# Optimization experiments

Measured on AMD Instinct MI355X. Metric: run time of the kernel, lower is better.

Reference implementation:

```python
import jax, jax.numpy as jnp
import numpy as np


def setup_inputs() -> dict:
    key = jax.random.key(0)
    kq, kk, kv, kiq, kik = jax.random.split(key, 5)
    B, H, S, D = 2, 16, 4096, 64
    NSQ = 2048  # round(0.5 * S)
    NSK = 2048  # round(0.5 * S)
    Q = jax.random.normal(kq, (B, H, S, D), dtype=jnp.float32)
    K = jax.random.normal(kk, (B, H, S, D), dtype=jnp.float32)
    V = jax.random.normal(kv, (B, H, S, D), dtype=jnp.float32)
    mask = jnp.ones((B, S), dtype=jnp.float32)
    sample_idx_q = jnp.sort(jax.random.randint(kiq, (NSQ,), 0, S, dtype=jnp.int32))
    sample_idx_k = jax.random.randint(kik, (NSK,), 0, S, dtype=jnp.int32)
    return {"Q": Q, "K": K, "V": V, "mask": mask,
            "sample_idx_q": sample_idx_q, "sample_idx_k": sample_idx_k}


def reference(Q, K, V, mask, sample_idx_q, sample_idx_k):
    # Q,K,V: [B,H,S,D]; sample_idx_q sorted int [NSQ]; sample_idx_k int [NSK]
    S = Q.shape[-2]
    nsq = sample_idx_q.shape[0]
    nsk = sample_idx_k.shape[0]
    Qs = Q[:, :, sample_idx_q, :]            # [B,H,NSQ,D]
    Vs = V[:, :, sample_idx_k, :]            # [B,H,NSK,D]
    # NOTE: original code computes K's softmax from Q (faithful to source bug):
    Qsm = jax.nn.softmax(Qs, axis=-1)        # softmax over head_dim
    Ksm = jax.nn.softmax(Qsm, axis=-2)       # softmax over sampled seq dim
    # dot = K^T @ V : [B,H,D,D]  (requires NSQ == NSK, as in source)
    dot = jnp.einsum('bhsd,bhse->bhde', Ksm, Vs)
    ac = jnp.einsum('bhsd,bhde->bhse', Qsm, dot)  # [B,H,NSQ,D]
    scale = (S * S) / (nsq * nsk)
    ac = scale * ac + (S / nsk) * Vs
    # Serial duplicate-merge + scatter == segmented sum over duplicate q indices,
    # written into a zero tensor at the unique sampled positions.
    attn = jnp.zeros_like(V).at[:, :, sample_idx_q, :].add(ac)
    return attn
```

## Files before the change

### kernel.cpp

```cpp
#include <hip/hip_runtime.h>

constexpr int S     = 4096;
constexpr int D     = 64;
constexpr int NSQ   = 2048;
constexpr int BH    = 32;
constexpr int SD    = S * D;
constexpr int SPLIT = 32;
constexpr int RPB   = NSQ / SPLIT;
constexpr int RPW   = RPB / 4;
constexpr int PE    = 66;
constexpr int PQ    = 68;

using f32x16 = __attribute__((ext_vector_type(16))) float;
using s16x8  = __attribute__((ext_vector_type(8)))  short;

#define DEV static __device__ __forceinline__

DEV unsigned short f2bf(float f) {
    unsigned x = __builtin_bit_cast(unsigned, f);
    x += 0x7fffu + ((x >> 16) & 1u);
    return (unsigned short)(x >> 16);
}

DEV float row_softmax(float q) {
    float mx = q;
    #pragma unroll
    for (int s = 32; s; s >>= 1) mx = fmaxf(mx, __shfl_xor(mx, s));
    float e = __expf(q - mx);
    float sm = e;
    #pragma unroll
    for (int s = 32; s; s >>= 1) sm += __shfl_xor(sm, s);
    return e / sm;
}

DEV s16x8 load_frag(const unsigned short* p) {
    const unsigned* u = (const unsigned*)p;
    union { unsigned w[4]; s16x8 v; } r;
    r.w[0] = u[0]; r.w[1] = u[1]; r.w[2] = u[2]; r.w[3] = u[3];
    return r.v;
}

__global__ __launch_bounds__(256) void
kA(const float* __restrict__ Q, const float* __restrict__ V,
   const int* __restrict__ iq, const int* __restrict__ ik,
   float* __restrict__ Mws, float* __restrict__ Cws) {
    __shared__ unsigned short Et[64 * PE];
    __shared__ unsigned short Vt[64 * PE];
    __shared__ float Cl[4][64];

    const int bh   = blockIdx.x / SPLIT;
    const int sp   = blockIdx.x % SPLIT;
    const int lane = threadIdx.x & 63;
    const int wave = threadIdx.x >> 6;

    const float* Qb = Q + (size_t)bh * SD;
    const float* Vb = V + (size_t)bh * SD;

    float c = 0.f;
    const int rbase = sp * RPB + wave * RPW;
    #pragma unroll 2
    for (int r = 0; r < RPW; ++r) {
        const int i  = rbase + r;
        const int qi = iq[i];
        const int ki = ik[i];
        const float q = Qb[qi * D + lane];
        const float v = Vb[ki * D + lane];
        const float qsm = row_softmax(q);
        const float ev  = __expf(qsm);
        c += ev;
        const int sl = wave * RPW + r;
        Et[lane * PE + sl] = f2bf(ev);
        Vt[lane * PE + sl] = f2bf(v);
    }
    Cl[wave][lane] = c;
    __syncthreads();

    const int d0 = (wave & 1) * 32, e0 = (wave >> 1) * 32;
    const int m  = lane & 31, h = lane >> 5;
    f32x16 acc = {0,0,0,0,0,0,0,0,0,0,0,0,0,0,0,0};
    #pragma unroll
    for (int t = 0; t < RPB / 16; ++t) {
        s16x8 a = load_frag(&Et[(d0 + m) * PE + t * 16 + h * 8]);
        s16x8 b = load_frag(&Vt[(e0 + m) * PE + t * 16 + h * 8]);
        acc = __builtin_amdgcn_mfma_f32_32x32x16_bf16(a, b, acc, 0, 0, 0);
    }

    float* Mb = Mws + bh * 4096;
    #pragma unroll
    for (int r = 0; r < 16; ++r) {
        const int row = (r & 3) + 8 * (r >> 2) + 4 * h;
        atomicAdd(&Mb[(d0 + row) * 64 + (e0 + m)], acc[r]);
    }
    if (wave == 0) {
        const float cs = Cl[0][lane] + Cl[1][lane] + Cl[2][lane] + Cl[3][lane];
        atomicAdd(&Cws[bh * 64 + lane], cs);
    }
}

__global__ __launch_bounds__(256) void
kC(const float* __restrict__ Q, const float* __restrict__ V,
   const int* __restrict__ iq, const int* __restrict__ ik,
   const float* __restrict__ Mws, const float* __restrict__ Cws,
   float* __restrict__ out) {
    __shared__ unsigned short Qs[RPB * PQ];
    __shared__ unsigned short Gt[64 * PQ];
    __shared__ int iqL[RPB];
    __shared__ int ikL[RPB];

    const int bh   = blockIdx.x / SPLIT;
    const int sp   = blockIdx.x % SPLIT;
    const int lane = threadIdx.x & 63;
    const int wave = threadIdx.x >> 6;

    const float* Mb = Mws + bh * 4096;
    const float* Cb = Cws + bh * 64;
    for (int t = threadIdx.x; t < 4096; t += 256) {
        const int d = t >> 6, e = t & 63;
        Gt[e * PQ + d] = f2bf(4.0f * Mb[t] / Cb[d]);
    }

    const float* Qb = Q + (size_t)bh * SD;
    const float* Vb = V + (size_t)bh * SD;
    float*       Ob = out + (size_t)bh * SD;
    const int rbase = sp * RPB;

    if (threadIdx.x < RPB) {
        iqL[threadIdx.x] = iq[rbase + threadIdx.x];
        ikL[threadIdx.x] = ik[rbase + threadIdx.x];
    }

    #pragma unroll 2
    for (int r = 0; r < RPW; ++r) {
        const int sl = wave * RPW + r;
        const int i  = rbase + sl;
        const int qi = iq[i];
        const float q = Qb[qi * D + lane];
        Qs[sl * PQ + lane] = f2bf(row_softmax(q));
    }
    __syncthreads();

    const int m0 = (wave & 1) * 32, n0 = (wave >> 1) * 32;
    const int m  = lane & 31, h = lane >> 5;

    f32x16 acc;
    #pragma unroll
    for (int r = 0; r < 16; ++r) {
        const int row = (r & 3) + 8 * (r >> 2) + 4 * h;
        const int ki  = ikL[m0 + row];
        acc[r] = 2.0f * Vb[ki * D + n0 + m];
    }
    #pragma unroll
    for (int t = 0; t < RPB / 16; ++t) {
        s16x8 a = load_frag(&Qs[(m0 + m) * PQ + t * 16 + h * 8]);
        s16x8 b = load_frag(&Gt[(n0 + m) * PQ + t * 16 + h * 8]);
        acc = __builtin_amdgcn_mfma_f32_32x32x16_bf16(a, b, acc, 0, 0, 0);
    }
    #pragma unroll
    for (int r = 0; r < 16; ++r) {
        const int row = (r & 3) + 8 * (r >> 2) + 4 * h;
        const int qi  = iqL[m0 + row];
        atomicAdd(&Ob[qi * D + n0 + m], acc[r]);
    }
}

extern "C" void kernel_launch(void* const* d_in, const int* in_sizes, int n_in,
                              void* d_out, int out_size, void* d_ws, size_t ws_size,
                              hipStream_t stream) {
    const float* Q  = (const float*)d_in[0];
    const float* V  = (const float*)d_in[2];
    const int*   iq = (const int*)d_in[4];
    const int*   ik = (const int*)d_in[5];
    float*       out = (float*)d_out;

    float* Mws = (float*)d_ws;
    float* Cws = Mws + BH * D * D;

    hipMemsetAsync(d_out, 0, (size_t)out_size * sizeof(float), stream);
    hipMemsetAsync(d_ws, 0, (size_t)(BH * D * D + BH * D) * sizeof(float), stream);

    kA<<<BH * SPLIT, 256, 0, stream>>>(Q, V, iq, ik, Mws, Cws);
    kC<<<BH * SPLIT, 256, 0, stream>>>(Q, V, iq, ik, Mws, Cws, out);
}
```

Measured before the change: 174.5 us.

## Replace atomic K^T V accumulation with per-split partials and vectorized softmax loads

kA now writes a per-split partial D×D matrix and column sums to workspace instead of using atomicAdd. kC sums those partials itself, which removes the workspace memset and the atomic contention. Both kernels now load Q and V rows as float4 with 16 lanes per row, computing the row softmax with a 4-step shuffle reduction instead of a full 64-lane reduce. kA uses 16 splits with 128 rows each, halving its block count. The cost is that every kC block redundantly reads all 16 partials (256 KB per bh), which adds L2 traffic.

```diff
diff --git a/kernel.cpp b/kernel.cpp
--- a/kernel.cpp
+++ b/kernel.cpp
@@ -1,15 +1,22 @@
 #include <hip/hip_runtime.h>
 
-constexpr int S     = 4096;
-constexpr int D     = 64;
-constexpr int NSQ   = 2048;
-constexpr int BH    = 32;
-constexpr int SD    = S * D;
-constexpr int SPLIT = 32;
-constexpr int RPB   = NSQ / SPLIT;
-constexpr int RPW   = RPB / 4;
-constexpr int PE    = 66;
-constexpr int PQ    = 68;
+constexpr int S    = 4096;
+constexpr int D    = 64;
+constexpr int NSQ  = 2048;
+constexpr int BH   = 32;
+constexpr int SD   = S * D;
+
+constexpr int SPA  = 16;
+constexpr int RPBA = NSQ / SPA;
+constexpr int RPWA = RPBA / 4;
+constexpr int ITA  = RPWA / 4;
+constexpr int PEA  = 130;
+
+constexpr int SPC  = 32;
+constexpr int RPBC = NSQ / SPC;
+constexpr int RPWC = RPBC / 4;
+constexpr int ITC  = RPWC / 4;
+constexpr int PQ   = 68;
 
 using f32x16 = __attribute__((ext_vector_type(16))) float;
 using s16x8  = __attribute__((ext_vector_type(8)))  short;
@@ -20,17 +27,6 @@
     unsigned x = __builtin_bit_cast(unsigned, f);
     x += 0x7fffu + ((x >> 16) & 1u);
     return (unsigned short)(x >> 16);
-}
-
-DEV float row_softmax(float q) {
-    float mx = q;
-    #pragma unroll
-    for (int s = 32; s; s >>= 1) mx = fmaxf(mx, __shfl_xor(mx, s));
-    float e = __expf(q - mx);
-    float sm = e;
-    #pragma unroll
-    for (int s = 32; s; s >>= 1) sm += __shfl_xor(sm, s);
-    return e / sm;
 }
 
 DEV s16x8 load_frag(const unsigned short* p) {
@@ -43,105 +39,161 @@
 __global__ __launch_bounds__(256) void
 kA(const float* __restrict__ Q, const float* __restrict__ V,
    const int* __restrict__ iq, const int* __restrict__ ik,
-   float* __restrict__ Mws, float* __restrict__ Cws) {
-    __shared__ unsigned short Et[64 * PE];
-    __shared__ unsigned short Vt[64 * PE];
-    __shared__ float Cl[4][64];
-
-    const int bh   = blockIdx.x / SPLIT;
-    const int sp   = blockIdx.x % SPLIT;
+   float* __restrict__ Mp, float* __restrict__ Cp) {
+    __shared__ unsigned short Et[64 * PEA];
+    __shared__ unsigned short Vt[64 * PEA];
+    __shared__ float Cl[4][256];
+    __shared__ int iqL[RPBA], ikL[RPBA];
+
+    const int bh   = blockIdx.x / SPA;
+    const int sp   = blockIdx.x % SPA;
     const int lane = threadIdx.x & 63;
     const int wave = threadIdx.x >> 6;
+    const int rq   = lane >> 4;
+    const int c    = lane & 15;
+
+    const int rbase = sp * RPBA;
+    if (threadIdx.x < RPBA) {
+        iqL[threadIdx.x] = iq[rbase + threadIdx.x];
+        ikL[threadIdx.x] = ik[rbase + threadIdx.x];
+    }
+    __syncthreads();
 
     const float* Qb = Q + (size_t)bh * SD;
     const float* Vb = V + (size_t)bh * SD;
 
-    float c = 0.f;
-    const int rbase = sp * RPB + wave * RPW;
-    #pragma unroll 2
-    for (int r = 0; r < RPW; ++r) {
-        const int i  = rbase + r;
-        const int qi = iq[i];
-        const int ki = ik[i];
-        const float q = Qb[qi * D + lane];
-        const float v = Vb[ki * D + lane];
-        const float qsm = row_softmax(q);
-        const float ev  = __expf(qsm);
-        c += ev;
-        const int sl = wave * RPW + r;
-        Et[lane * PE + sl] = f2bf(ev);
-        Vt[lane * PE + sl] = f2bf(v);
-    }
-    Cl[wave][lane] = c;
-    __syncthreads();
-
-    const int d0 = (wave & 1) * 32, e0 = (wave >> 1) * 32;
+    float c4[4] = {0.f, 0.f, 0.f, 0.f};
+    #pragma unroll
+    for (int it = 0; it < ITA; ++it) {
+        const int sl = wave * RPWA + it * 4 + rq;
+        const int qi = iqL[sl];
+        const int ki = ikL[sl];
+        const float4 qv = *(const float4*)&Qb[qi * D + 4 * c];
+        const float4 vv = *(const float4*)&Vb[ki * D + 4 * c];
+        const float e0 = __expf(qv.x), e1 = __expf(qv.y),
+                    e2 = __expf(qv.z), e3 = __expf(qv.w);
+        float s = (e0 + e1) + (e2 + e3);
+        s += __shfl_xor(s, 1); s += __shfl_xor(s, 2);
+        s += __shfl_xor(s, 4); s += __shfl_xor(s, 8);
+        const float inv = 1.0f / s;
+        const float E0 = __expf(e0 * inv), E1 = __expf(e1 * inv),
+                    E2 = __expf(e2 * inv), E3 = __expf(e3 * inv);
+        c4[0] += E0; c4[1] += E1; c4[2] += E2; c4[3] += E3;
+        Et[(4 * c + 0) * PEA + sl] = f2bf(E0);
+        Et[(4 * c + 1) * PEA + sl] = f2bf(E1);
+        Et[(4 * c + 2) * PEA + sl] = f2bf(E2);
+        Et[(4 * c + 3) * PEA + sl] = f2bf(E3);
+        Vt[(4 * c + 0) * PEA + sl] = f2bf(vv.x);
+        Vt[(4 * c + 1) * PEA + sl] = f2bf(vv.y);
+        Vt[(4 * c + 2) * PEA + sl] = f2bf(vv.z);
+        Vt[(4 * c + 3) * PEA + sl] = f2bf(vv.w);
+    }
+    Cl[wave][lane * 4 + 0] = c4[0];
+    Cl[wave][lane * 4 + 1] = c4[1];
+    Cl[wave][lane * 4 + 2] = c4[2];
+    Cl[wave][lane * 4 + 3] = c4[3];
+    __syncthreads();
+
+    const int d0 = (wave & 1) * 32, n0 = (wave >> 1) * 32;
     const int m  = lane & 31, h = lane >> 5;
     f32x16 acc = {0,0,0,0,0,0,0,0,0,0,0,0,0,0,0,0};
     #pragma unroll
-    for (int t = 0; t < RPB / 16; ++t) {
-        s16x8 a = load_frag(&Et[(d0 + m) * PE + t * 16 + h * 8]);
-        s16x8 b = load_frag(&Vt[(e0 + m) * PE + t * 16 + h * 8]);
+    for (int t = 0; t < RPBA / 16; ++t) {
+        s16x8 a = load_frag(&Et[(d0 + m) * PEA + t * 16 + h * 8]);
+        s16x8 b = load_frag(&Vt[(n0 + m) * PEA + t * 16 + h * 8]);
         acc = __builtin_amdgcn_mfma_f32_32x32x16_bf16(a, b, acc, 0, 0, 0);
     }
 
-    float* Mb = Mws + bh * 4096;
+    float* Mb = Mp + ((size_t)bh * SPA + sp) * 4096;
     #pragma unroll
     for (int r = 0; r < 16; ++r) {
         const int row = (r & 3) + 8 * (r >> 2) + 4 * h;
-        atomicAdd(&Mb[(d0 + row) * 64 + (e0 + m)], acc[r]);
+        Mb[(d0 + row) * 64 + n0 + m] = acc[r];
     }
     if (wave == 0) {
-        const float cs = Cl[0][lane] + Cl[1][lane] + Cl[2][lane] + Cl[3][lane];
-        atomicAdd(&Cws[bh * 64 + lane], cs);
+        const int cc = lane >> 2, j = lane & 3;
+        float cs = 0.f;
+        #pragma unroll
+        for (int w = 0; w < 4; ++w)
+            #pragma unroll
+            for (int r = 0; r < 4; ++r)
+                cs += Cl[w][(16 * r + cc) * 4 + j];
+        Cp[((size_t)bh * SPA + sp) * 64 + lane] = cs;
     }
 }
 
 __global__ __launch_bounds__(256) void
 kC(const float* __restrict__ Q, const float* __restrict__ V,
    const int* __restrict__ iq, const int* __restrict__ ik,
-   const float* __restrict__ Mws, const float* __restrict__ Cws,
+   const float* __restrict__ Mp, const float* __restrict__ Cp,
    float* __restrict__ out) {
-    __shared__ unsigned short Qs[RPB * PQ];
+    __shared__ unsigned short Qs[RPBC * PQ];
     __shared__ unsigned short Gt[64 * PQ];
-    __shared__ int iqL[RPB];
-    __shared__ int ikL[RPB];
-
-    const int bh   = blockIdx.x / SPLIT;
-    const int sp   = blockIdx.x % SPLIT;
+    __shared__ float Cf[64];
+    __shared__ int iqL[RPBC], ikL[RPBC];
+
+    const int bh   = blockIdx.x / SPC;
+    const int sp   = blockIdx.x % SPC;
     const int lane = threadIdx.x & 63;
     const int wave = threadIdx.x >> 6;
-
-    const float* Mb = Mws + bh * 4096;
-    const float* Cb = Cws + bh * 64;
-    for (int t = threadIdx.x; t < 4096; t += 256) {
-        const int d = t >> 6, e = t & 63;
-        Gt[e * PQ + d] = f2bf(4.0f * Mb[t] / Cb[d]);
+    const int rq   = lane >> 4;
+    const int c    = lane & 15;
+
+    const int rbase = sp * RPBC;
+    if (threadIdx.x < RPBC) {
+        iqL[threadIdx.x] = iq[rbase + threadIdx.x];
+        ikL[threadIdx.x] = ik[rbase + threadIdx.x];
+    }
+    if (threadIdx.x < 64) {
+        float cs = 0.f;
+        #pragma unroll
+        for (int p = 0; p < SPA; ++p)
+            cs += Cp[((size_t)bh * SPA + p) * 64 + threadIdx.x];
+        Cf[threadIdx.x] = cs;
+    }
+    __syncthreads();
+
+    const float* MpB = Mp + (size_t)bh * SPA * 4096;
+    #pragma unroll
+    for (int k = 0; k < 4; ++k) {
+        const int elb = (k * 256 + threadIdx.x) * 4;
+        const int d = elb >> 6, e4 = elb & 63;
+        float4 ms = {0.f, 0.f, 0.f, 0.f};
+        #pragma unroll
+        for (int p = 0; p < SPA; ++p) {
+            const float4 t = *(const float4*)&MpB[p * 4096 + elb];
+            ms.x += t.x; ms.y += t.y; ms.z += t.z; ms.w += t.w;
+        }
+        const float g = 4.0f / Cf[d];
+        Gt[(e4 + 0) * PQ + d] = f2bf(ms.x * g);
+        Gt[(e4 + 1) * PQ + d] = f2bf(ms.y * g);
+        Gt[(e4 + 2) * PQ + d] = f2bf(ms.z * g);
+        Gt[(e4 + 3) * PQ + d] = f2bf(ms.w * g);
     }
 
     const float* Qb = Q + (size_t)bh * SD;
     const float* Vb = V + (size_t)bh * SD;
     float*       Ob = out + (size_t)bh * SD;
-    const int rbase = sp * RPB;
-
-    if (threadIdx.x < RPB) {
-        iqL[threadIdx.x] = iq[rbase + threadIdx.x];
-        ikL[threadIdx.x] = ik[rbase + threadIdx.x];
-    }
-
-    #pragma unroll 2
-    for (int r = 0; r < RPW; ++r) {
-        const int sl = wave * RPW + r;
-        const int i  = rbase + sl;
-        const int qi = iq[i];
-        const float q = Qb[qi * D + lane];
-        Qs[sl * PQ + lane] = f2bf(row_softmax(q));
+    #pragma unroll
+    for (int it = 0; it < ITC; ++it) {
+        const int sl = wave * RPWC + it * 4 + rq;
+        const int qi = iqL[sl];
+        const float4 qv = *(const float4*)&Qb[qi * D + 4 * c];
+        const float e0 = __expf(qv.x), e1 = __expf(qv.y),
+                    e2 = __expf(qv.z), e3 = __expf(qv.w);
+        float s = (e0 + e1) + (e2 + e3);
+        s += __shfl_xor(s, 1); s += __shfl_xor(s, 2);
+        s += __shfl_xor(s, 4); s += __shfl_xor(s, 8);
+        const float inv = 1.0f / s;
+        uint2 pk;
+        pk.x = (unsigned)f2bf(e0 * inv) | ((unsigned)f2bf(e1 * inv) << 16);
+        pk.y = (unsigned)f2bf(e2 * inv) | ((unsigned)f2bf(e3 * inv) << 16);
+        *(uint2*)&Qs[sl * PQ + 4 * c] = pk;
     }
     __syncthreads();
 
     const int m0 = (wave & 1) * 32, n0 = (wave >> 1) * 32;
     const int m  = lane & 31, h = lane >> 5;
-
     f32x16 acc;
     #pragma unroll
     for (int r = 0; r < 16; ++r) {
@@ -150,7 +202,7 @@
         acc[r] = 2.0f * Vb[ki * D + n0 + m];
     }
     #pragma unroll
-    for (int t = 0; t < RPB / 16; ++t) {
+    for (int t = 0; t < RPBC / 16; ++t) {
         s16x8 a = load_frag(&Qs[(m0 + m) * PQ + t * 16 + h * 8]);
         s16x8 b = load_frag(&Gt[(n0 + m) * PQ + t * 16 + h * 8]);
         acc = __builtin_amdgcn_mfma_f32_32x32x16_bf16(a, b, acc, 0, 0, 0);
@@ -172,12 +224,10 @@
     const int*   ik = (const int*)d_in[5];
     float*       out = (float*)d_out;
 
-    float* Mws = (float*)d_ws;
-    float* Cws = Mws + BH * D * D;
+    float* Mp = (float*)d_ws;
+    float* Cp = Mp + (size_t)BH * SPA * 4096;
 
     hipMemsetAsync(d_out, 0, (size_t)out_size * sizeof(float), stream);
-    hipMemsetAsync(d_ws, 0, (size_t)(BH * D * D + BH * D) * sizeof(float), stream);
-
-    kA<<<BH * SPLIT, 256, 0, stream>>>(Q, V, iq, ik, Mws, Cws);
-    kC<<<BH * SPLIT, 256, 0, stream>>>(Q, V, iq, ik, Mws, Cws, out);
-}
+    kA<<<BH * SPA, 256, 0, stream>>>(Q, V, iq, ik, Mp, Cp);
+    kC<<<BH * SPC, 256, 0, stream>>>(Q, V, iq, ik, Mp, Cp, out);
+}
```

Result: faster. 155.8 us (-10.7%).
